# Performance work log

Hardware: AMD Instinct MI355X
Metric: run time of the kernel (lower is better)

## Reference

```python
import jax, jax.numpy as jnp
import numpy as np

POP_SIZE = 4096
OUT_SIZE = 256
CODON_SIZE = 8  # log2(OUT_SIZE)
N_BLOCKS = 36


def _make_building_blocks():
    # Mirrors KroneckerGATorch.generate_building_block_tensor:
    # diag in {-1,0,1}, upper in {0,1}, lower in {-1,0} -> 3*3*2*2 = 36 blocks
    blocks = []
    for i in range(3):
        for j in range(3):
            for k in range(2):
                for l in range(2):
                    blocks.append([[i - 1, k], [l - 1, j - 1]])
    return jnp.asarray(np.array(blocks, dtype=np.float32))  # [36, 2, 2]


def setup_inputs() -> dict:
    key = jax.random.key(0)
    kw, ki = jax.random.split(key)
    weights = jax.random.normal(kw, (POP_SIZE,), dtype=jnp.float32)
    indices = jax.random.randint(ki, (POP_SIZE, CODON_SIZE), 0, N_BLOCKS)
    building_blocks = _make_building_blocks()
    return {"weights": weights, "indices": indices, "building_blocks": building_blocks}


def reference(weights, indices, building_blocks):
    # Batched geno2pheno over the whole population.
    # blocks: [P, C, 2, 2] gathered building blocks per genome codon
    blocks = building_blocks[indices]
    P = blocks.shape[0]
    # Iteratively expand the Kronecker product across codons (fixed C=8 loop).
    # kron(A, B)[i*2+k, j*2+l] = A[i,j] * B[k,l]
    kp = jnp.ones((P, 1, 1), dtype=blocks.dtype)
    for c in range(CODON_SIZE):
        s = kp.shape[-1]
        kp = jnp.einsum("pij,pkl->pikjl", kp, blocks[:, c]).reshape(P, 2 * s, 2 * s)
    # Weighted accumulation over the population -> [OUT_SIZE, OUT_SIZE]
    return jnp.einsum("p,pij->ij", weights, kp)
```

## Files before the change

kernel.cpp:

```cpp
#include <hip/hip_runtime.h>


#define Z_CHUNKS 32
#define LDK 136

typedef __attribute__((ext_vector_type(8))) short bf16x8;
typedef __attribute__((ext_vector_type(4))) float f32x4;

__device__ __forceinline__ short f32_to_bf16(float f) {
    unsigned u = __float_as_uint(f);
    u = u + 0x7FFFu + ((u >> 16) & 1u);
    return (short)(u >> 16);
}

__device__ __forceinline__ void decode_block(int d, float2& r0, float2& r1) {
    const int l  = d & 1;
    const int k  = (d >> 1) & 1;
    const int ij = d >> 2;
    const int i  = (ij * 11) >> 5;
    const int j  = ij - 3 * i;
    r0.x = (float)(i - 1); r0.y = (float)k;
    r1.x = (float)(l - 1); r1.y = (float)(j - 1);
}

__device__ __forceinline__ void stage_side(const int4 gi, int ibase, int q, int g,
                                           short* sDst, short posb, short negb) {
    float2 a0, a1, b0, b1, c0, c1, d0, d1;
    decode_block(gi.x, a0, a1);
    decode_block(gi.y, b0, b1);
    decode_block(gi.z, c0, c1);
    decode_block(gi.w, d0, d1);
#pragma unroll
    for (int t = 0; t < 2; ++t) {
        const int cg = q * 2 + t;
        const int i1 = ibase + cg;
        const float2 s0 = ((i1 >> 3) & 1) ? a1 : a0;
        const float2 s1 = ((i1 >> 2) & 1) ? b1 : b0;
        const float2 s2 = ((i1 >> 1) & 1) ? c1 : c0;
        const float2 s3 = ((i1     ) & 1) ? d1 : d0;
        float P01[4], P23[4];
        P01[0] = s0.x * s1.x; P01[1] = s0.x * s1.y;
        P01[2] = s0.y * s1.x; P01[3] = s0.y * s1.y;
        P23[0] = s2.x * s3.x; P23[1] = s2.x * s3.y;
        P23[2] = s2.y * s3.x; P23[3] = s2.y * s3.y;
        short* col = sDst + (cg * 16) * LDK + g;
#pragma unroll
        for (int cc = 0; cc < 16; ++cc) {
            const float prod = P01[cc >> 2] * P23[cc & 3];
            const short v = prod > 0.5f ? posb : (prod < -0.5f ? negb : (short)0);
            col[cc * LDK] = v;
        }
    }
}

__global__ __launch_bounds__(256) void kron_ga_partial(
    const float* __restrict__ weights,
    const int*   __restrict__ indices,
    const float* __restrict__ bb,
    float*       __restrict__ ws)
{
    __shared__ short sA[64 * LDK];
    __shared__ short sB[64 * LDK];
    (void)bb;

    const int tid = threadIdx.x;
    const int m0  = blockIdx.y * 64;
    const int n0  = blockIdx.x * 64;
    const int pbase = blockIdx.z * 128;

    {
        const int g = tid & 127;
        const int q = tid >> 7;
        const int p = pbase + g;
        const int4 lo = *(const int4*)&indices[p * 8];
        const int4 hi = *(const int4*)&indices[p * 8 + 4];
        const float w = weights[p];
        const short wb = f32_to_bf16(w);
        stage_side(lo, m0 >> 4, q, g, sA, wb, (short)(wb ^ (short)0x8000));
        stage_side(hi, n0 >> 4, q, g, sB, (short)0x3F80, (short)0xBF80);
    }
    __syncthreads();

    const int lane = tid & 63;
    const int lrow = lane & 15;
    const int quad = lane >> 4;
    const int wv   = tid >> 6;

    f32x4 acc[4] = {};
    const short* aBase = &sA[(wv * 16 + lrow) * LDK + quad * 8];
    const short* bBase = &sB[lrow * LDK + quad * 8];

#pragma unroll
    for (int ks = 0; ks < 128; ks += 32) {
        const bf16x8 af = *(const bf16x8*)(aBase + ks);
#pragma unroll
        for (int nt = 0; nt < 4; ++nt) {
            const bf16x8 bfr = *(const bf16x8*)(bBase + nt * 16 * LDK + ks);
            acc[nt] = __builtin_amdgcn_mfma_f32_16x16x32_bf16(af, bfr, acc[nt], 0, 0, 0);
        }
    }

    float* wsz = ws + (size_t)blockIdx.z * (256 * 256);
#pragma unroll
    for (int nt = 0; nt < 4; ++nt) {
#pragma unroll
        for (int r = 0; r < 4; ++r) {
            const int mm = m0 + wv * 16 + quad * 4 + r;
            const int nn = n0 + nt * 16 + lrow;
            wsz[mm * 256 + nn] = acc[nt][r];
        }
    }
}

__global__ __launch_bounds__(256) void kron_ga_reduce(
    const float* __restrict__ ws,
    float*       __restrict__ out)
{
    const int o = blockIdx.x * 256 + threadIdx.x;
    float s = 0.f;
#pragma unroll
    for (int z = 0; z < Z_CHUNKS; ++z)
        s += ws[(size_t)z * (256 * 256) + o];
    const int mm = o >> 8, nn = o & 255;
    const int i1 = mm >> 4, j1 = mm & 15;
    const int i2 = nn >> 4, j2 = nn & 15;
    out[((i1 * 16 + i2) << 8) + j1 * 16 + j2] = s;
}

extern "C" void kernel_launch(void* const* d_in, const int* in_sizes, int n_in,
                              void* d_out, int out_size, void* d_ws, size_t ws_size,
                              hipStream_t stream) {
    const float* weights = (const float*)d_in[0];
    const int*   indices = (const int*)d_in[1];
    const float* bb      = (const float*)d_in[2];
    float* out = (float*)d_out;
    float* ws  = (float*)d_ws;

    dim3 grid1(4, 4, Z_CHUNKS);
    kron_ga_partial<<<grid1, 256, 0, stream>>>(weights, indices, bb, ws);

    kron_ga_reduce<<<256, 256, 0, stream>>>(ws, out);
}
```

Measured before the change: 64.32 us.

## Fuse partial GEMM and reduction into one-pass kernel per output tile

Replaces the two-kernel scheme (partial products written to a workspace for 32 population chunks, then a separate reduce kernel) with a single kernel. Each of 256 blocks owns one 16x16 output tile and loops over the full population in 1024-genome chunks. It stages swizzled bf16 factor columns in shared memory and reduces the per-wave MFMA accumulators in shared memory before writing the output. This removes the workspace round trip and the second launch, at the cost of a serial loop over chunks with two barriers per chunk and a long K dimension per block.

```diff
diff --git a/kernel.cpp b/kernel.cpp
--- a/kernel.cpp
+++ b/kernel.cpp
@@ -1,8 +1,8 @@
 #include <hip/hip_runtime.h>
 
 
-#define Z_CHUNKS 32
-#define LDK 136
+#define CHUNK 1024
+#define NCHUNK 4
 
 typedef __attribute__((ext_vector_type(8))) short bf16x8;
 typedef __attribute__((ext_vector_type(4))) float f32x4;
@@ -13,118 +13,105 @@
     return (short)(u >> 16);
 }
 
-__device__ __forceinline__ void decode_block(int d, float2& r0, float2& r1) {
+__device__ __forceinline__ float2 decode_row(int d, int rb) {
     const int l  = d & 1;
     const int k  = (d >> 1) & 1;
     const int ij = d >> 2;
     const int i  = (ij * 11) >> 5;
     const int j  = ij - 3 * i;
-    r0.x = (float)(i - 1); r0.y = (float)k;
-    r1.x = (float)(l - 1); r1.y = (float)(j - 1);
+    float2 r;
+    r.x = (float)(rb ? (l - 1) : (i - 1));
+    r.y = (float)(rb ? (j - 1) : k);
+    return r;
 }
 
-__device__ __forceinline__ void stage_side(const int4 gi, int ibase, int q, int g,
-                                           short* sDst, short posb, short negb) {
-    float2 a0, a1, b0, b1, c0, c1, d0, d1;
-    decode_block(gi.x, a0, a1);
-    decode_block(gi.y, b0, b1);
-    decode_block(gi.z, c0, c1);
-    decode_block(gi.w, d0, d1);
-#pragma unroll
-    for (int t = 0; t < 2; ++t) {
-        const int cg = q * 2 + t;
-        const int i1 = ibase + cg;
-        const float2 s0 = ((i1 >> 3) & 1) ? a1 : a0;
-        const float2 s1 = ((i1 >> 2) & 1) ? b1 : b0;
-        const float2 s2 = ((i1 >> 1) & 1) ? c1 : c0;
-        const float2 s3 = ((i1     ) & 1) ? d1 : d0;
-        float P01[4], P23[4];
-        P01[0] = s0.x * s1.x; P01[1] = s0.x * s1.y;
-        P01[2] = s0.y * s1.x; P01[3] = s0.y * s1.y;
-        P23[0] = s2.x * s3.x; P23[1] = s2.x * s3.y;
-        P23[2] = s2.y * s3.x; P23[3] = s2.y * s3.y;
-        short* col = sDst + (cg * 16) * LDK + g;
-#pragma unroll
-        for (int cc = 0; cc < 16; ++cc) {
-            const float prod = P01[cc >> 2] * P23[cc & 3];
-            const short v = prod > 0.5f ? posb : (prod < -0.5f ? negb : (short)0);
-            col[cc * LDK] = v;
-        }
-    }
-}
-
-__global__ __launch_bounds__(256) void kron_ga_partial(
+__global__ __launch_bounds__(512) void kron_ga_onepass(
     const float* __restrict__ weights,
     const int*   __restrict__ indices,
     const float* __restrict__ bb,
-    float*       __restrict__ ws)
+    float*       __restrict__ out)
 {
-    __shared__ short sA[64 * LDK];
-    __shared__ short sB[64 * LDK];
+    __shared__ short sAB[2 * 16 * CHUNK];
     (void)bb;
 
-    const int tid = threadIdx.x;
-    const int m0  = blockIdx.y * 64;
-    const int n0  = blockIdx.x * 64;
-    const int pbase = blockIdx.z * 128;
-
-    {
-        const int g = tid & 127;
-        const int q = tid >> 7;
-        const int p = pbase + g;
-        const int4 lo = *(const int4*)&indices[p * 8];
-        const int4 hi = *(const int4*)&indices[p * 8 + 4];
-        const float w = weights[p];
-        const short wb = f32_to_bf16(w);
-        stage_side(lo, m0 >> 4, q, g, sA, wb, (short)(wb ^ (short)0x8000));
-        stage_side(hi, n0 >> 4, q, g, sB, (short)0x3F80, (short)0xBF80);
-    }
-    __syncthreads();
-
+    const int tid  = threadIdx.x;
+    const int side = tid >> 8;
+    const int tg   = tid & 255;
+    const int gl   = tg * 4;
+    const int wv   = tid >> 6;
     const int lane = tid & 63;
     const int lrow = lane & 15;
     const int quad = lane >> 4;
-    const int wv   = tid >> 6;
+    const int by   = (int)blockIdx.x >> 4;
+    const int bx   = (int)blockIdx.x & 15;
+    const int rsel = side ? bx : by;
+    const int cofs = side ? 4 : 0;
+    short* const sSide = sAB + side * (16 * CHUNK);
 
-    f32x4 acc[4] = {};
-    const short* aBase = &sA[(wv * 16 + lrow) * LDK + quad * 8];
-    const short* bBase = &sB[lrow * LDK + quad * 8];
+    f32x4 acc = {};
 
+    for (int ch = 0; ch < NCHUNK; ++ch) {
+        {
+            float P01[4][4], P23[4][4];
 #pragma unroll
-    for (int ks = 0; ks < 128; ks += 32) {
-        const bf16x8 af = *(const bf16x8*)(aBase + ks);
+            for (int gg = 0; gg < 4; ++gg) {
+                const int p = ch * CHUNK + gl + gg;
+                const int4 gi = *(const int4*)&indices[p * 8 + cofs];
+                float2 v0 = decode_row(gi.x, (rsel >> 3) & 1);
+                float2 v1 = decode_row(gi.y, (rsel >> 2) & 1);
+                float2 v2 = decode_row(gi.z, (rsel >> 1) & 1);
+                float2 v3 = decode_row(gi.w, rsel & 1);
+                if (side == 0) {
+                    const short wb = f32_to_bf16(weights[p]);
+                    const float wf =
+                        __uint_as_float(((unsigned)(unsigned short)wb) << 16);
+                    v0.x *= wf; v0.y *= wf;
+                }
+                P01[gg][0] = v0.x * v1.x; P01[gg][1] = v0.x * v1.y;
+                P01[gg][2] = v0.y * v1.x; P01[gg][3] = v0.y * v1.y;
+                P23[gg][0] = v2.x * v3.x; P23[gg][1] = v2.x * v3.y;
+                P23[gg][2] = v2.y * v3.x; P23[gg][3] = v2.y * v3.y;
+            }
 #pragma unroll
-        for (int nt = 0; nt < 4; ++nt) {
-            const bf16x8 bfr = *(const bf16x8*)(bBase + nt * 16 * LDK + ks);
-            acc[nt] = __builtin_amdgcn_mfma_f32_16x16x32_bf16(af, bfr, acc[nt], 0, 0, 0);
+            for (int c = 0; c < 16; ++c) {
+                const float e0 = P01[0][c >> 2] * P23[0][c & 3];
+                const float e1 = P01[1][c >> 2] * P23[1][c & 3];
+                const float e2 = P01[2][c >> 2] * P23[2][c & 3];
+                const float e3 = P01[3][c >> 2] * P23[3][c & 3];
+                const unsigned lo = __builtin_amdgcn_perm(
+                    __float_as_uint(e1), __float_as_uint(e0), 0x07060302u);
+                const unsigned hi = __builtin_amdgcn_perm(
+                    __float_as_uint(e3), __float_as_uint(e2), 0x07060302u);
+                const int blk = (gl >> 3) ^ (c & 7);
+                const int idx = c * CHUNK + blk * 8 + (gl & 7);
+                *(uint2*)&sSide[idx] = make_uint2(lo, hi);
+            }
         }
+        __syncthreads();
+
+        const short* sA = sAB;
+        const short* sB = sAB + 16 * CHUNK;
+#pragma unroll
+        for (int ks = 0; ks < 4; ++ks) {
+            const int blk  = wv * 16 + ks * 4 + quad;
+            const int sblk = blk ^ (lrow & 7);
+            const bf16x8 af = *(const bf16x8*)&sA[lrow * CHUNK + sblk * 8];
+            const bf16x8 bf = *(const bf16x8*)&sB[lrow * CHUNK + sblk * 8];
+            acc = __builtin_amdgcn_mfma_f32_16x16x32_bf16(af, bf, acc, 0, 0, 0);
+        }
+        __syncthreads();
     }
 
-    float* wsz = ws + (size_t)blockIdx.z * (256 * 256);
+    float* comb = (float*)sAB;
+    *(f32x4*)&comb[wv * 256 + lrow * 16 + quad * 4] = acc;
+    __syncthreads();
+    if (tid < 256) {
+        float s = 0.f;
 #pragma unroll
-    for (int nt = 0; nt < 4; ++nt) {
-#pragma unroll
-        for (int r = 0; r < 4; ++r) {
-            const int mm = m0 + wv * 16 + quad * 4 + r;
-            const int nn = n0 + nt * 16 + lrow;
-            wsz[mm * 256 + nn] = acc[nt][r];
-        }
+        for (int w = 0; w < 8; ++w)
+            s += comb[w * 256 + (tid & 15) * 16 + (tid >> 4)];
+        out[((int)blockIdx.x << 8) + tid] = s;
     }
-}
-
-__global__ __launch_bounds__(256) void kron_ga_reduce(
-    const float* __restrict__ ws,
-    float*       __restrict__ out)
-{
-    const int o = blockIdx.x * 256 + threadIdx.x;
-    float s = 0.f;
-#pragma unroll
-    for (int z = 0; z < Z_CHUNKS; ++z)
-        s += ws[(size_t)z * (256 * 256) + o];
-    const int mm = o >> 8, nn = o & 255;
-    const int i1 = mm >> 4, j1 = mm & 15;
-    const int i2 = nn >> 4, j2 = nn & 15;
-    out[((i1 * 16 + i2) << 8) + j1 * 16 + j2] = s;
 }
 
 extern "C" void kernel_launch(void* const* d_in, const int* in_sizes, int n_in,
@@ -134,10 +121,7 @@
     const int*   indices = (const int*)d_in[1];
     const float* bb      = (const float*)d_in[2];
     float* out = (float*)d_out;
-    float* ws  = (float*)d_ws;
+    (void)d_ws; (void)ws_size;
 
-    dim3 grid1(4, 4, Z_CHUNKS);
-    kron_ga_partial<<<grid1, 256, 0, stream>>>(weights, indices, bb, ws);
-
-    kron_ga_reduce<<<256, 256, 0, stream>>>(ws, out);
+    kron_ga_onepass<<<256, 512, 0, stream>>>(weights, indices, bb, out);
 }
```

Result: slower. 66.70 us (+3.7%).
